# Performance work log

Hardware: AMD Instinct MI355X
Metric: run time of the kernel (lower is better)

Reference implementation:

```python
import jax, jax.numpy as jnp
import numpy as np
from jax import lax

B, T_ENC, T_DEC, D, MEL, PRE = 64, 300, 500, 512, 80, 256
K, C_LOC = 31, 32


def setup_inputs() -> dict:
    key = jax.random.key(0)
    ks = iter(jax.random.split(key, 40))
    def w(shape, s=0.05):
        return jax.random.normal(next(ks), shape, dtype=jnp.float32) * s
    zb = lambda n: jnp.zeros((n,), jnp.float32)
    return {
        "enc": w((B, T_ENC, D), 1.0),
        "mel_in": w((B, T_DEC, MEL), 1.0),
        "prenet_w1": w((PRE, MEL)), "prenet_b1": zb(PRE),
        "prenet_w2": w((PRE, PRE)), "prenet_b2": zb(PRE),
        "att_wih": w((4 * D, D + PRE)), "att_whh": w((4 * D, D)),
        "att_bih": zb(4 * D), "att_bhh": zb(4 * D),
        "dec_wih": w((4 * D, 2 * D)), "dec_whh": w((4 * D, D)),
        "dec_bih": zb(4 * D), "dec_bhh": zb(4 * D),
        "q_w": w((D, D)), "q_b": zb(D),
        "mem_w": w((D, D)), "mem_b": zb(D),
        "loc_conv_w": w((C_LOC, 2, K)), "loc_conv_b": zb(C_LOC),
        "loc_proj_w": w((D, C_LOC)), "loc_proj_b": zb(D),
        "v_w": w((1, D)), "v_b": zb(1),
        "mel_w": w((MEL, D)), "mel_b": zb(MEL),
        "stop_w": w((1, D)), "stop_b": zb(1),
    }


def _lstm(x, h, c, wih, whh, bih, bhh):
    # torch.nn.LSTMCell math: gates = x W_ih^T + b_ih + h W_hh^T + b_hh
    g = x @ wih.T + bih + h @ whh.T + bhh
    i, f, gg, o = jnp.split(g, 4, axis=-1)
    c = jax.nn.sigmoid(f) * c + jax.nn.sigmoid(i) * jnp.tanh(gg)
    h = jax.nn.sigmoid(o) * jnp.tanh(c)
    return h, c


def reference(enc, mel_in, prenet_w1, prenet_b1, prenet_w2, prenet_b2,
              att_wih, att_whh, att_bih, att_bhh,
              dec_wih, dec_whh, dec_bih, dec_bhh,
              q_w, q_b, mem_w, mem_b,
              loc_conv_w, loc_conv_b, loc_proj_w, loc_proj_b,
              v_w, v_b, mel_w, mel_b, stop_w, stop_b):
    # Eval mode (dropout/zoneout off), teacher_forcing=1.0 -> prev_mel = mel_in[:, t].
    Bb, T_enc, Dd = enc.shape
    pad = (loc_conv_w.shape[-1] - 1) // 2
    mproj = enc @ mem_w.T + mem_b  # [B, T_enc, D] (hoisted; constant across steps)

    def step(carry, prev_mel):
        ctx, a, a_cum, h_att, c_att, h_dec, c_dec = carry
        # prenet: two Linear+ReLU (dropout off in eval)
        pm = jax.nn.relu(jax.nn.relu(prev_mel @ prenet_w1.T + prenet_b1) @ prenet_w2.T + prenet_b2)
        h_att, c_att = _lstm(jnp.concatenate([pm, ctx], -1), h_att, c_att,
                             att_wih, att_whh, att_bih, att_bhh)
        # location-sensitive attention
        loc = jnp.stack([a, a_cum], axis=1)  # [B, 2, T_enc]
        conv = lax.conv_general_dilated(loc, loc_conv_w, (1,), [(pad, pad)],
                                        dimension_numbers=("NCH", "OIH", "NCH"))
        conv = conv + loc_conv_b[None, :, None]  # [B, C_loc, T_enc]
        loc_feat = jnp.einsum("bct,dc->btd", conv, loc_proj_w) + loc_proj_b  # [B, T_enc, D]
        q = (h_att @ q_w.T + q_b)[:, None, :]  # [B, 1, D]
        e = jnp.tanh(q + mproj + loc_feat) @ v_w[0] + v_b[0]  # [B, T_enc]
        a = jax.nn.softmax(e, axis=1)
        ctx = jnp.einsum("bt,btd->bd", a, enc)
        a_cum = a_cum + a
        h_dec, c_dec = _lstm(jnp.concatenate([h_att, ctx], -1), h_dec, c_dec,
                             dec_wih, dec_whh, dec_bih, dec_bhh)
        mel = h_dec @ mel_w.T + mel_b          # [B, mel_dim]
        stop = h_dec @ stop_w[0] + stop_b[0]   # [B]
        return (ctx, a, a_cum, h_att, c_att, h_dec, c_dec), (mel, stop)

    z = lambda *s: jnp.zeros(s, enc.dtype)
    init = (z(Bb, Dd), z(Bb, T_enc), z(Bb, T_enc), z(Bb, Dd), z(Bb, Dd), z(Bb, Dd), z(Bb, Dd))
    _, (mels, stops) = lax.scan(step, init, jnp.swapaxes(mel_in, 0, 1))
    mel_out = jnp.swapaxes(mels, 0, 1)    # [B, T_dec, mel_dim]
    stop_out = jnp.swapaxes(stops, 0, 1)  # [B, T_dec]
    return mel_out, stop_out
```

## Files before the change

### kernel.cpp

```cpp
#include <hip/hip_runtime.h>
#include <hip/hip_bf16.h>


#define DEV __device__ __forceinline__
typedef __hip_bfloat16 bf16;
DEV float b2f(bf16 x) { return __bfloat162float(x); }
DEV unsigned short f2us(float f) { bf16 h = __float2bfloat16(f); unsigned short u; __builtin_memcpy(&u, &h, 2); return u; }
DEV float us2f(unsigned short u) { union { float f; unsigned int i; } c; c.i = ((unsigned)u) << 16; return c.f; }

constexpr int NB = 256;

__device__ float g_enc[64*300*512];
__device__ __align__(16) float g_melT[500*80*64];
__device__ __align__(16) float g_w1[256*80];
__device__ float g_b1[256];
__device__ __align__(16) float g_w2[256*256];
__device__ float g_b2[256];
__device__ __align__(16) float g_awih[2048*768];
__device__ __align__(16) float g_awhh[2048*512];
__device__ float g_ab[2048];
__device__ __align__(16) float g_dwih[2048*1024];
__device__ __align__(16) float g_dwhh[2048*512];
__device__ float g_db[2048];
__device__ __align__(16) float g_qwt[512*512];
__device__ float g_qpb[512];
__device__ __align__(16) float g_memwt[512*512];
__device__ float g_memb[512];
__device__ float g_cw[32*62];
__device__ float g_cb[32];
__device__ __align__(16) float g_pw[512*32];
__device__ float g_vw[512];
__device__ __align__(16) float g_melw[80*512];
__device__ float g_melb[80];
__device__ __align__(16) float g_stopw[512];
__device__ float g_scal[2];
__device__ int   g_f32io;
__device__ __align__(16) float g_hatt4[2*512*64];
__device__ __align__(16) float g_hattT[64*512];
__device__ float g_catt[512*64];
__device__ __align__(16) float g_hdec4[2*512*64];
__device__ float g_cdec[512*64];
__device__ __align__(16) float g_ctx4[512*64];
__device__ float g_a[64*300];
__device__ float g_acum[64*300];
__device__ __align__(16) float g_pmt4[256*64];
__device__ __align__(16) float g_pm1t4[256*64];
__device__ float g_e[64*300];
__device__ int g_flag[NB*32];
__device__ int g_go[16*32];

struct InPtrs { const void* p[28]; };

DEV float sigf(float x) { return 1.f / (1.f + __expf(-x)); }
DEV float tanhf_fast(float x) {
  float e = __expf(-2.f * fabsf(x));
  float r = (1.f - e) / (1.f + e);
  return copysignf(r, x);
}
DEV int zero_vgpr() { int z; asm volatile("v_mov_b32 %0, 0" : "=v"(z)); return z; }

DEV float ald(const float* p) {
  return __hip_atomic_load(p, __ATOMIC_RELAXED, __HIP_MEMORY_SCOPE_AGENT);
}
DEV void ast(float* p, float v) {
  __hip_atomic_store(p, v, __ATOMIC_RELAXED, __HIP_MEMORY_SCOPE_AGENT);
}
DEV float2 ald2(const float* p) {
  unsigned long long u = __hip_atomic_load((const unsigned long long*)p,
                                           __ATOMIC_RELAXED, __HIP_MEMORY_SCOPE_AGENT);
  union { unsigned long long u; float2 f; } c; c.u = u; return c.f;
}

DEV int detect_f32(const void* enc_raw) {
  const unsigned short* u = (const unsigned short*)enc_raw;
  int big = 0;
  for (int i = 0; i < 256; i += 2) { int e = (u[i] >> 7) & 0xFF; big += (e > 133) ? 1 : 0; }
  return big >= 8 ? 1 : 0;
}
DEV float ldin(const void* p, int i, int f32) {
  return f32 ? ((const float*)p)[i] : b2f(((const bf16*)p)[i]);
}

__global__ __launch_bounds__(256) void k_convert(InPtrs P) {
  const int NT = gridDim.x * 256;
  const int flat = blockIdx.x * 256 + threadIdx.x;
  const int f32 = detect_f32(P.p[0]);
  if (flat == 0) {
    g_f32io = f32;
    g_scal[0] = ldin(P.p[23], 0, f32);
    g_scal[1] = ldin(P.p[27], 0, f32);
  }
#define CVT(dst, idx, n) for (int i = flat; i < (n); i += NT) dst[i] = ldin(P.p[idx], i, f32);
  CVT(g_enc, 0, 64*300*512)
  CVT(g_w1, 2, 256*80)   CVT(g_b1, 3, 256)
  CVT(g_w2, 4, 256*256)  CVT(g_b2, 5, 256)
  CVT(g_awih, 6, 2048*768)  CVT(g_awhh, 7, 2048*512)
  CVT(g_dwih, 10, 2048*1024) CVT(g_dwhh, 11, 2048*512)
  CVT(g_cw, 18, 32*62) CVT(g_cb, 19, 32)
  CVT(g_pw, 20, 512*32)  CVT(g_vw, 22, 512)
  CVT(g_melw, 24, 80*512) CVT(g_melb, 25, 80)
  CVT(g_stopw, 26, 512)  CVT(g_memb, 17, 512)
#undef CVT
  for (int i = flat; i < 500*80*64; i += NT) {
    int b = i & 63, tm = i >> 6;
    g_melT[i] = ldin(P.p[1], b*40000 + tm, f32);
  }
  for (int i = flat; i < 2048; i += NT) g_ab[i] = ldin(P.p[8], i, f32) + ldin(P.p[9], i, f32);
  for (int i = flat; i < 2048; i += NT) g_db[i] = ldin(P.p[12], i, f32) + ldin(P.p[13], i, f32);
  for (int i = flat; i < 512; i += NT) g_qpb[i] = ldin(P.p[15], i, f32) + ldin(P.p[21], i, f32);
  for (int o = flat; o < 512*512; o += NT) {
    int d = o >> 9, k = o & 511;
    g_memwt[(size_t)k*512 + d] = ldin(P.p[16], o, f32);
    g_qwt[(size_t)k*512 + d]   = ldin(P.p[14], o, f32);
  }
  for (int i = flat; i < 2*512*64; i += NT) { g_hatt4[i] = 0.f; g_hdec4[i] = 0.f; }
  for (int i = flat; i < 512*64; i += NT) { g_catt[i] = 0.f; g_cdec[i] = 0.f; g_ctx4[i] = 0.f; }
  for (int i = flat; i < 64*512; i += NT) g_hattT[i] = 0.f;
  for (int i = flat; i < 64*300; i += NT) { g_a[i] = 0.f; g_acum[i] = 0.f; }
  for (int i = flat; i < NB*32; i += NT) g_flag[i] = 0;
  for (int i = flat; i < 16*32; i += NT) g_go[i] = 0;
}

DEV void gbar(int n, int bb, int tid) {
  asm volatile("s_waitcnt vmcnt(0) lgkmcnt(0)" ::: "memory");
  __syncthreads();
  if (tid == 0)
    __hip_atomic_store(&g_flag[bb*32], n, __ATOMIC_RELAXED, __HIP_MEMORY_SCOPE_AGENT);
  if (bb == 0) {
    if (tid < 256)
      while (__hip_atomic_load(&g_flag[tid*32], __ATOMIC_RELAXED, __HIP_MEMORY_SCOPE_AGENT) < n)
        __builtin_amdgcn_s_sleep(1);
    __syncthreads();
    if (tid < 16)
      __hip_atomic_store(&g_go[tid*32], n, __ATOMIC_RELAXED, __HIP_MEMORY_SCOPE_AGENT);
  } else {
    if (tid == 0) {
      while (__hip_atomic_load(&g_go[(bb>>4)*32], __ATOMIC_RELAXED, __HIP_MEMORY_SCOPE_AGENT) < n)
        __builtin_amdgcn_s_sleep(1);
    }
  }
  __syncthreads();
}

template<int RS>
DEV void pdot16(const float* __restrict__ X4, const float* __restrict__ W0,
                int bbu, int k0, int nk, int lane, float* acc) {
#pragma unroll 2
  for (int k = k0; k < k0 + nk; k += 8) {
    const float* xp = X4 + k*64 + lane*4;
    float2 xa0 = ald2(xp);
    float2 xb0 = ald2(xp + 2);
    float2 xa1 = ald2(xp + 256);
    float2 xb1 = ald2(xp + 258);
#pragma unroll
    for (int g = 0; g < 4; ++g) {
#pragma unroll
      for (int u = 0; u < 4; ++u) {
        const float* wp = W0 + (size_t)(g*512 + bbu*4 + u)*RS + k;
        float4 w0 = *(const float4*)(wp);
        float4 w1 = *(const float4*)(wp + 4);
        float a = acc[g*4+u];
        a = fmaf(w0.x, xa0.x, a); a = fmaf(w0.y, xa0.y, a);
        a = fmaf(w0.z, xb0.x, a); a = fmaf(w0.w, xb0.y, a);
        a = fmaf(w1.x, xa1.x, a); a = fmaf(w1.y, xa1.y, a);
        a = fmaf(w1.z, xb1.x, a); a = fmaf(w1.w, xb1.y, a);
        acc[g*4+u] = a;
      }
    }
  }
}

DEV float dotSg(const float* __restrict__ X4, const float* __restrict__ wr,
                int n, int lane, float acc) {
#pragma unroll 2
  for (int k = 0; k < n; k += 8) {
    const float* xp = X4 + k*64 + lane*4;
    float2 xa0 = ald2(xp);
    float2 xb0 = ald2(xp + 2);
    float2 xa1 = ald2(xp + 256);
    float2 xb1 = ald2(xp + 258);
    float4 u0 = *(const float4*)(wr + k);
    float4 u1 = *(const float4*)(wr + k + 4);
    acc = fmaf(u0.x, xa0.x, acc); acc = fmaf(u0.y, xa0.y, acc);
    acc = fmaf(u0.z, xb0.x, acc); acc = fmaf(u0.w, xb0.y, acc);
    acc = fmaf(u1.x, xa1.x, acc); acc = fmaf(u1.y, xa1.y, acc);
    acc = fmaf(u1.z, xb1.x, acc); acc = fmaf(u1.w, xb1.y, acc);
  }
  return acc;
}

__global__ __launch_bounds__(512) void k_dec(void* outv) {
  const int bb = blockIdx.x;
  const int tid = threadIdx.x;
  const int lane = tid & 63, wv = tid >> 6;
  const int h = wv >> 2, dwv = wv & 3;
  const int f32io = g_f32io;
  const int zi = zero_vgpr();
  bf16* outh = (bf16*)outv;
  float* outf = (float*)outv;

  __shared__ __align__(16) float sbuf[8192];
  __shared__ float part[8][40];
  __shared__ float s_h[512];
  __shared__ float s_aa[664];
  __shared__ float s_cw[2016];

  const int eb = bb >> 2, tt0 = (bb & 3) * 75;
  const int da = dwv*128 + lane*2;
  const int r0 = h*38, nr = 38 - h;
  int bn = 0;

  for (int i = tid; i < 1984; i += 512) s_cw[i] = g_cw[i];
  for (int i = tid; i < 32; i += 512) s_cw[1984 + i] = g_cb[i];
  for (int i = tid; i < 664; i += 512) s_aa[i] = 0.f;
  __syncthreads();

  const int bbu = (bb < 128) ? bb : (bb - 128);
  const int jrow = bbu*4 + dwv;
  float bi, bfg, bgg, bog;
  if (bb < 128) { bi = g_ab[jrow]; bfg = g_ab[512+jrow]; bgg = g_ab[1024+jrow]; bog = g_ab[1536+jrow]; }
  else          { bi = g_db[jrow]; bfg = g_db[512+jrow]; bgg = g_db[1024+jrow]; bog = g_db[1536+jrow]; }
  float prb = 0.f;
  if (bb >= 128 && bb < 148) prb = g_melb[(bb-128)*4 + dwv];
  else if (bb >= 64 && bb < 128) prb = g_b2[(bb-64)*4 + dwv];
  else if (bb >= 192) prb = g_b1[(bb-192)*4 + dwv];

  if (bb >= 192 && tid < 256) {
    float acc = prb;
    const float* mt = g_melT + lane;
    const float* wr = g_w1 + zi + (size_t)((bb-192)*4 + dwv)*80;
#pragma unroll
    for (int m4 = 0; m4 < 20; ++m4) {
      float4 w = *(const float4*)(wr + m4*4);
      acc = fmaf(w.x, mt[(m4*4+0)*64], acc);
      acc = fmaf(w.y, mt[(m4*4+1)*64], acc);
      acc = fmaf(w.z, mt[(m4*4+2)*64], acc);
      acc = fmaf(w.w, mt[(m4*4+3)*64], acc);
    }
    ast(&g_pm1t4[(bb-192)*256 + lane*4 + dwv], fmaxf(acc, 0.f));
  }
  gbar(++bn, bb, tid);

  unsigned int mpq[38];
  {
    float a1[38], a2[38];
#pragma unroll
    for (int r = 0; r < 38; ++r) { a1[r] = 0.f; a2[r] = 0.f; }
    for (int kt = 0; kt < 16; ++kt) {
      __syncthreads();
      for (int i = tid; i < 75*32; i += 512) {
        int r = i >> 5, kk = i & 31;
        sbuf[i] = g_enc[((size_t)eb*300 + tt0 + r)*512 + kt*32 + kk];
      }
      __syncthreads();
      for (int kk = 0; kk < 32; ++kk) {
        const int k = kt*32 + kk;
        const float2 w = *(const float2*)(g_memwt + (size_t)k*512 + da);
#pragma unroll
        for (int r = 0; r < 38; ++r) {
          const float ev = sbuf[(r0 + r)*32 + kk];
          a1[r] = fmaf(ev, w.x, a1[r]);
          a2[r] = fmaf(ev, w.y, a2[r]);
        }
      }
    }
    const float2 mb = *(const float2*)(g_memb + da);
#pragma unroll
    for (int r = 0; r < 38; ++r)
      mpq[r] = (unsigned)f2us(a1[r] + mb.x) | ((unsigned)f2us(a2[r] + mb.y) << 16);
    if (bb >= 64 && bb < 128 && wv < 4) {
      float acc = dotSg(g_pm1t4, g_w2 + zi + (size_t)((bb-64)*4 + dwv)*256, 256, lane, prb);
      ast(&g_pmt4[(bb-64)*256 + lane*4 + dwv], fmaxf(acc, 0.f));
    }
  }
  float Pa[32], Pb[32];
#pragma unroll
  for (int i = 0; i < 8; ++i) {
    float4 u = *(const float4*)(g_pw + (size_t)da*32 + 4*i);
    float4 w = *(const float4*)(g_pw + (size_t)(da+1)*32 + 4*i);
    Pa[4*i] = u.x; Pa[4*i+1] = u.y; Pa[4*i+2] = u.z; Pa[4*i+3] = u.w;
    Pb[4*i] = w.x; Pb[4*i+1] = w.y; Pb[4*i+2] = w.z; Pb[4*i+3] = w.w;
  }
  const float2 vv  = *(const float2*)(g_vw + da);
  const float2 qb2 = *(const float2*)(g_qpb + da);
  const float v1 = vv.x, v2 = vv.y;
  const float vb = g_scal[0];
  gbar(++bn, bb, tid);

  for (int t = 0; t <= 500; ++t) {
    const int rp = t & 1, wp = rp ^ 1;

    if (bb < 128) {
      if (t < 500) {
        float acc[16];
#pragma unroll
        for (int r = 0; r < 16; ++r) acc[r] = 0.f;
        pdot16<768>(g_pmt4, g_awih + zi, bb, wv*32, 32, lane, acc);
        pdot16<768>(g_ctx4, g_awih + zi + 256, bb, wv*64, 64, lane, acc);
        pdot16<512>(g_hatt4 + rp*(512*64), g_awhh + zi, bb, wv*64, 64, lane, acc);
#pragma unroll
        for (int r = 0; r < 16; ++r) sbuf[r*512 + wv*64 + lane] = acc[r];
        __syncthreads();
        if (wv < 4) {
          float s0 = bi, s1 = bfg, s2 = bgg, s3 = bog;
#pragma unroll
          for (int w = 0; w < 8; ++w) {
            s0 += sbuf[(dwv)*512      + w*64 + lane];
            s1 += sbuf[(4 + dwv)*512  + w*64 + lane];
            s2 += sbuf[(8 + dwv)*512  + w*64 + lane];
            s3 += sbuf[(12 + dwv)*512 + w*64 + lane];
          }
          const float c = g_catt[jrow*64 + lane];
          const float cn = sigf(s1)*c + sigf(s0)*tanhf_fast(s2);
          const float hn = sigf(s3)*tanhf_fast(cn);
          g_catt[jrow*64 + lane] = cn;
          ast(&g_hatt4[wp*(512*64) + bb*256 + lane*4 + dwv], hn);
          ast(&g_hattT[lane*512 + jrow], hn);
        }
      }
    } else {
      if (t > 0) {
        float acc[16];
#pragma unroll
        for (int r = 0; r < 16; ++r) acc[r] = 0.f;
        pdot16<1024>(g_hatt4 + rp*(512*64), g_dwih + zi, bbu, wv*64, 64, lane, acc);
        pdot16<1024>(g_ctx4, g_dwih + zi + 512, bbu, wv*64, 64, lane, acc);
        pdot16<512>(g_hdec4 + wp*(512*64), g_dwhh + zi, bbu, wv*64, 64, lane, acc);
#pragma unroll
        for (int r = 0; r < 16; ++r) sbuf[r*512 + wv*64 + lane] = acc[r];
        __syncthreads();
        if (wv < 4) {
          float s0 = bi, s1 = bfg, s2 = bgg, s3 = bog;
#pragma unroll
          for (int w = 0; w < 8; ++w) {
            s0 += sbuf[(dwv)*512      + w*64 + lane];
            s1 += sbuf[(4 + dwv)*512  + w*64 + lane];
            s2 += sbuf[(8 + dwv)*512  + w*64 + lane];
            s3 += sbuf[(12 + dwv)*512 + w*64 + lane];
          }
          const float c = g_cdec[jrow*64 + lane];
          const float cn = sigf(s1)*c + sigf(s0)*tanhf_fast(s2);
          const float hn = sigf(s3)*tanhf_fast(cn);
          g_cdec[jrow*64 + lane] = cn;
          ast(&g_hdec4[rp*(512*64) + (bb-128)*256 + lane*4 + dwv], hn);
        }
      }
    }
    gbar(++bn, bb, tid);

    if (t < 500) {
      s_h[tid] = ald(&g_hattT[eb*512 + tid]);
      if (tid < 300) {
        s_aa[15 + tid]  = ald(&g_a[eb*300 + tid]);
        s_aa[347 + tid] = ald(&g_acum[eb*300 + tid]);
      }
      __syncthreads();
      for (int i = tid; i < 75*32; i += 512) {
        const int ttl = i >> 5, c2 = i & 31;
        const int tt = tt0 + ttl;
        float s = s_cw[1984 + c2];
#pragma unroll
        for (int k = 0; k < 31; ++k) {
          s = fmaf(s_cw[c2*62 + k],      s_aa[tt + k], s);
          s = fmaf(s_cw[c2*62 + 31 + k], s_aa[332 + tt + k], s);
        }
        sbuf[i] = s;
      }
      float q1p = h ? 0.f : qb2.x, q2p = h ? 0.f : qb2.y;
      {
        const int kb = h*256;
#pragma unroll 8
        for (int k = kb; k < kb + 256; k += 2) {
          const float h0 = s_h[k], h1 = s_h[k+1];
          const float2 wA = *(const float2*)(g_qwt + (size_t)k*512 + da);
          const float2 wB = *(const float2*)(g_qwt + (size_t)(k+1)*512 + da);
          q1p = fmaf(wA.x, h0, q1p); q2p = fmaf(wA.y, h0, q2p);
          q1p = fmaf(wB.x, h1, q1p); q2p = fmaf(wB.y, h1, q2p);
        }
      }
      float2* qp = (float2*)(sbuf + 4096);
      qp[wv*64 + lane] = make_float2(q1p, q2p);
      __syncthreads();
      const float2 qA = qp[dwv*64 + lane];
      const float2 qB = qp[(4 + dwv)*64 + lane];
      const float q1 = qA.x + qB.x, q2 = qA.y + qB.y;
#pragma unroll
      for (int i = 0; i < 38; ++i) {
        if (i < nr) {
          const int gi = r0 + i;
          float s1 = q1 + us2f((unsigned short)(mpq[i] & 0xffffu));
          float s2 = q2 + us2f((unsigned short)(mpq[i] >> 16));
          const float4* cr = (const float4*)(sbuf + gi*32);
#pragma unroll
          for (int c4 = 0; c4 < 8; ++c4) {
            const float4 cv = cr[c4];
            s1 = fmaf(Pa[c4*4+0], cv.x, s1); s2 = fmaf(Pb[c4*4+0], cv.x, s2);
            s1 = fmaf(Pa[c4*4+1], cv.y, s1); s2 = fmaf(Pb[c4*4+1], cv.y, s2);
            s1 = fmaf(Pa[c4*4+2], cv.z, s1); s2 = fmaf(Pb[c4*4+2], cv.z, s2);
            s1 = fmaf(Pa[c4*4+3], cv.w, s1); s2 = fmaf(Pb[c4*4+3], cv.w, s2);
          }
          float p = v1*tanhf_fast(s1) + v2*tanhf_fast(s2);
#pragma unroll
          for (int m = 32; m >= 1; m >>= 1) p += __shfl_xor(p, m, 64);
          if (lane == 0) part[wv][i] = p;
        }
      }
      __syncthreads();
      if (tid < 75) {
        float e;
        if (tid < 38) e = part[0][tid] + part[1][tid] + part[2][tid] + part[3][tid];
        else          e = part[4][tid-38] + part[5][tid-38] + part[6][tid-38] + part[7][tid-38];
        ast(&g_e[eb*300 + tt0 + tid], e + vb);
      }
    }
    if (t <= 498 && bb >= 192 && tid < 256) {
      float acc = prb;
      const float* mt = g_melT + (size_t)(t+1)*5120 + lane;
      const float* wr = g_w1 + zi + (size_t)((bb-192)*4 + dwv)*80;
#pragma unroll
      for (int m4 = 0; m4 < 20; ++m4) {
        float4 w = *(const float4*)(wr + m4*4);
        acc = fmaf(w.x, mt[(m4*4+0)*64], acc);
        acc = fmaf(w.y, mt[(m4*4+1)*64], acc);
        acc = fmaf(w.z, mt[(m4*4+2)*64], acc);
        acc = fmaf(w.w, mt[(m4*4+3)*64], acc);
      }
      ast(&g_pm1t4[(bb-192)*256 + lane*4 + dwv], fmaxf(acc, 0.f));
    }
    gbar(++bn, bb, tid);

    if (t < 500) {
      if (bb < 64) {
        float* pl = sbuf; float* red = sbuf + 304;
        const int b_ = bb;
        const float* Ep = g_e + b_*300;
        const float e1 = (tid < 300) ? ald(Ep + tid) : -3e38f;
        red[tid] = e1; __syncthreads();
        for (int s = 256; s > 0; s >>= 1) { if (tid < s) red[tid] = fmaxf(red[tid], red[tid+s]); __syncthreads(); }
        const float mx = red[0]; __syncthreads();
        const float p1 = (tid < 300) ? __expf(e1 - mx) : 0.f;
        if (tid < 300) pl[tid] = p1;
        red[tid] = p1; __syncthreads();
        for (int s = 256; s > 0; s >>= 1) { if (tid < s) red[tid] += red[tid+s]; __syncthreads(); }
        const float inv = 1.f / red[0];
        if (tid < 300) {
          const float av = p1*inv;
          const float oc = ald(&g_acum[b_*300 + tid]);
          ast(&g_a[b_*300 + tid], av);
          ast(&g_acum[b_*300 + tid], oc + av);
        }
        __syncthreads();
        const float* ep = g_enc + (size_t)(b_*300)*512;
        const int dd = tid;
        float acc = 0.f;
#pragma unroll 8
        for (int tt = 0; tt < 300; ++tt) acc = fmaf(pl[tt], ep[(size_t)tt*512 + dd], acc);
        ast(&g_ctx4[(dd >> 2)*256 + b_*4 + (dd & 3)], acc * inv);
      } else if (bb < 128) {
        if (t <= 498 && wv < 4) {
          float acc = dotSg(g_pm1t4, g_w2 + zi + (size_t)((bb-64)*4 + dwv)*256, 256, lane, prb);
          ast(&g_pmt4[(bb-64)*256 + lane*4 + dwv], fmaxf(acc, 0.f));
        }
      }
    }
    if (t > 0 && bb >= 128 && bb < 148 && wv < 4) {
      float acc = dotSg(g_hdec4 + rp*(512*64),
                        g_melw + zi + (size_t)((bb-128)*4 + dwv)*512, 512, lane, prb);
      const int m = (bb-128)*4 + dwv;
      const size_t oidx = (size_t)(lane*500 + (t-1))*80 + m;
      if (f32io) outf[oidx] = acc; else outh[oidx] = __float2bfloat16(acc);
    } else if (t > 0 && bb == 148 && tid < 64) {
      float acc = dotSg(g_hdec4 + rp*(512*64), g_stopw + zi, 512, tid, g_scal[1]);
      const size_t oidx = 2560000 + tid*500 + (t-1);
      if (f32io) outf[oidx] = acc; else outh[oidx] = __float2bfloat16(acc);
    }
    gbar(++bn, bb, tid);
  }
}

extern "C" void kernel_launch(void* const* d_in, const int* in_sizes, int n_in,
                              void* d_out, int out_size, void* d_ws, size_t ws_size,
                              hipStream_t stream) {
  (void)d_ws; (void)ws_size; (void)in_sizes; (void)out_size;
  InPtrs P;
  for (int i = 0; i < 28 && i < n_in; ++i) P.p[i] = d_in[i];
  k_convert<<<dim3(2048), dim3(256), 0, stream>>>(P);
  k_dec<<<dim3(NB), dim3(512), 0, stream>>>(d_out);
}
```

Before: 111.0 ms.

## Batch x-vector loads in LSTM dots, tile location conv, pipeline context loads

Several micro-optimizations to the persistent decoder kernel. pdot16 now loads all x chunks up front (fully unrolled) before the FMA loop, so more memory requests are in flight. The location conv is register-tiled with 5 outputs per thread, and the attention-weight smem loads are hoisted before the LSTM phase. The context reduction double-buffers the encoder loads with two accumulators. Removing the zero_vgpr trick lets weight pointers become scalar again, and the q projection uses float2 LDS loads. The cost is higher register pressure that could reduce occupancy or cause spills.

Result: slower. 200.5 ms (+80.7%).

```diff
diff --git a/kernel.cpp b/kernel.cpp
--- a/kernel.cpp
+++ b/kernel.cpp
@@ -57,7 +57,6 @@
   float r = (1.f - e) / (1.f + e);
   return copysignf(r, x);
 }
-DEV int zero_vgpr() { int z; asm volatile("v_mov_b32 %0, 0" : "=v"(z)); return z; }
 
 DEV float ald(const float* p) {
   return __hip_atomic_load(p, __ATOMIC_RELAXED, __HIP_MEMORY_SCOPE_AGENT);
@@ -142,16 +141,21 @@
   __syncthreads();
 }
 
-template<int RS>
+template<int RS, int NC>
 DEV void pdot16(const float* __restrict__ X4, const float* __restrict__ W0,
-                int bbu, int k0, int nk, int lane, float* acc) {
-#pragma unroll 2
-  for (int k = k0; k < k0 + nk; k += 8) {
-    const float* xp = X4 + k*64 + lane*4;
-    float2 xa0 = ald2(xp);
-    float2 xb0 = ald2(xp + 2);
-    float2 xa1 = ald2(xp + 256);
-    float2 xb1 = ald2(xp + 258);
+                int bbu, int k0, int lane, float* acc) {
+  float2 xr[NC*4];
+#pragma unroll
+  for (int c = 0; c < NC; ++c) {
+    const float* xp = X4 + (k0 + c*8)*64 + lane*4;
+    xr[c*4+0] = ald2(xp);
+    xr[c*4+1] = ald2(xp + 2);
+    xr[c*4+2] = ald2(xp + 256);
+    xr[c*4+3] = ald2(xp + 258);
+  }
+#pragma unroll
+  for (int c = 0; c < NC; ++c) {
+    const int k = k0 + c*8;
 #pragma unroll
     for (int g = 0; g < 4; ++g) {
 #pragma unroll
@@ -160,10 +164,10 @@
         float4 w0 = *(const float4*)(wp);
         float4 w1 = *(const float4*)(wp + 4);
         float a = acc[g*4+u];
-        a = fmaf(w0.x, xa0.x, a); a = fmaf(w0.y, xa0.y, a);
-        a = fmaf(w0.z, xb0.x, a); a = fmaf(w0.w, xb0.y, a);
-        a = fmaf(w1.x, xa1.x, a); a = fmaf(w1.y, xa1.y, a);
-        a = fmaf(w1.z, xb1.x, a); a = fmaf(w1.w, xb1.y, a);
+        a = fmaf(w0.x, xr[c*4+0].x, a); a = fmaf(w0.y, xr[c*4+0].y, a);
+        a = fmaf(w0.z, xr[c*4+1].x, a); a = fmaf(w0.w, xr[c*4+1].y, a);
+        a = fmaf(w1.x, xr[c*4+2].x, a); a = fmaf(w1.y, xr[c*4+2].y, a);
+        a = fmaf(w1.z, xr[c*4+3].x, a); a = fmaf(w1.w, xr[c*4+3].y, a);
         acc[g*4+u] = a;
       }
     }
@@ -195,14 +199,13 @@
   const int lane = tid & 63, wv = tid >> 6;
   const int h = wv >> 2, dwv = wv & 3;
   const int f32io = g_f32io;
-  const int zi = zero_vgpr();
   bf16* outh = (bf16*)outv;
   float* outf = (float*)outv;
 
   __shared__ __align__(16) float sbuf[8192];
   __shared__ float part[8][40];
   __shared__ float s_h[512];
-  __shared__ float s_aa[664];
+  __shared__ float s_aa[704];
   __shared__ float s_cw[2016];
 
   const int eb = bb >> 2, tt0 = (bb & 3) * 75;
@@ -212,7 +215,7 @@
 
   for (int i = tid; i < 1984; i += 512) s_cw[i] = g_cw[i];
   for (int i = tid; i < 32; i += 512) s_cw[1984 + i] = g_cb[i];
-  for (int i = tid; i < 664; i += 512) s_aa[i] = 0.f;
+  for (int i = tid; i < 704; i += 512) s_aa[i] = 0.f;
   __syncthreads();
 
   const int bbu = (bb < 128) ? bb : (bb - 128);
@@ -228,7 +231,7 @@
   if (bb >= 192 && tid < 256) {
     float acc = prb;
     const float* mt = g_melT + lane;
-    const float* wr = g_w1 + zi + (size_t)((bb-192)*4 + dwv)*80;
+    const float* wr = g_w1 + (size_t)((bb-192)*4 + dwv)*80;
 #pragma unroll
     for (int m4 = 0; m4 < 20; ++m4) {
       float4 w = *(const float4*)(wr + m4*4);
@@ -269,7 +272,7 @@
     for (int r = 0; r < 38; ++r)
       mpq[r] = (unsigned)f2us(a1[r] + mb.x) | ((unsigned)f2us(a2[r] + mb.y) << 16);
     if (bb >= 64 && bb < 128 && wv < 4) {
-      float acc = dotSg(g_pm1t4, g_w2 + zi + (size_t)((bb-64)*4 + dwv)*256, 256, lane, prb);
+      float acc = dotSg(g_pm1t4, g_w2 + (size_t)((bb-64)*4 + dwv)*256, 256, lane, prb);
       ast(&g_pmt4[(bb-64)*256 + lane*4 + dwv], fmaxf(acc, 0.f));
     }
   }
@@ -290,14 +293,18 @@
   for (int t = 0; t <= 500; ++t) {
     const int rp = t & 1, wp = rp ^ 1;
 
+    if (t < 500 && tid < 300) {
+      s_aa[15 + tid]  = ald(&g_a[eb*300 + tid]);
+      s_aa[347 + tid] = ald(&g_acum[eb*300 + tid]);
+    }
     if (bb < 128) {
       if (t < 500) {
         float acc[16];
 #pragma unroll
         for (int r = 0; r < 16; ++r) acc[r] = 0.f;
-        pdot16<768>(g_pmt4, g_awih + zi, bb, wv*32, 32, lane, acc);
-        pdot16<768>(g_ctx4, g_awih + zi + 256, bb, wv*64, 64, lane, acc);
-        pdot16<512>(g_hatt4 + rp*(512*64), g_awhh + zi, bb, wv*64, 64, lane, acc);
+        pdot16<768,4>(g_pmt4, g_awih, bb, wv*32, lane, acc);
+        pdot16<768,8>(g_ctx4, g_awih + 256, bb, wv*64, lane, acc);
+        pdot16<512,8>(g_hatt4 + rp*(512*64), g_awhh, bb, wv*64, lane, acc);
 #pragma unroll
         for (int r = 0; r < 16; ++r) sbuf[r*512 + wv*64 + lane] = acc[r];
         __syncthreads();
@@ -323,9 +330,9 @@
         float acc[16];
 #pragma unroll
         for (int r = 0; r < 16; ++r) acc[r] = 0.f;
-        pdot16<1024>(g_hatt4 + rp*(512*64), g_dwih + zi, bbu, wv*64, 64, lane, acc);
-        pdot16<1024>(g_ctx4, g_dwih + zi + 512, bbu, wv*64, 64, lane, acc);
-        pdot16<512>(g_hdec4 + wp*(512*64), g_dwhh + zi, bbu, wv*64, 64, lane, acc);
+        pdot16<1024,8>(g_hatt4 + rp*(512*64), g_dwih, bbu, wv*64, lane, acc);
+        pdot16<1024,8>(g_ctx4, g_dwih + 512, bbu, wv*64, lane, acc);
+        pdot16<512,8>(g_hdec4 + wp*(512*64), g_dwhh, bbu, wv*64, lane, acc);
 #pragma unroll
         for (int r = 0; r < 16; ++r) sbuf[r*512 + wv*64 + lane] = acc[r];
         __syncthreads();
@@ -350,32 +357,39 @@
 
     if (t < 500) {
       s_h[tid] = ald(&g_hattT[eb*512 + tid]);
-      if (tid < 300) {
-        s_aa[15 + tid]  = ald(&g_a[eb*300 + tid]);
-        s_aa[347 + tid] = ald(&g_acum[eb*300 + tid]);
-      }
       __syncthreads();
-      for (int i = tid; i < 75*32; i += 512) {
-        const int ttl = i >> 5, c2 = i & 31;
-        const int tt = tt0 + ttl;
-        float s = s_cw[1984 + c2];
-#pragma unroll
+      {
+        const int c2 = tid & 31, tb = tid >> 5;
+        const float cb0 = s_cw[1984 + c2];
+        float sc[5];
+#pragma unroll
+        for (int j = 0; j < 5; ++j) sc[j] = cb0;
         for (int k = 0; k < 31; ++k) {
-          s = fmaf(s_cw[c2*62 + k],      s_aa[tt + k], s);
-          s = fmaf(s_cw[c2*62 + 31 + k], s_aa[332 + tt + k], s);
-        }
-        sbuf[i] = s;
+          const float w1 = s_cw[c2*62 + k];
+          const float w2 = s_cw[c2*62 + 31 + k];
+          const int base = tt0 + tb + k;
+#pragma unroll
+          for (int j = 0; j < 5; ++j) {
+            sc[j] = fmaf(w1, s_aa[base + 16*j], sc[j]);
+            sc[j] = fmaf(w2, s_aa[332 + base + 16*j], sc[j]);
+          }
+        }
+#pragma unroll
+        for (int j = 0; j < 5; ++j) {
+          const int row = tb + 16*j;
+          if (row < 75) sbuf[row*32 + c2] = sc[j];
+        }
       }
       float q1p = h ? 0.f : qb2.x, q2p = h ? 0.f : qb2.y;
       {
         const int kb = h*256;
 #pragma unroll 8
         for (int k = kb; k < kb + 256; k += 2) {
-          const float h0 = s_h[k], h1 = s_h[k+1];
+          const float2 hh = *(const float2*)(s_h + k);
           const float2 wA = *(const float2*)(g_qwt + (size_t)k*512 + da);
           const float2 wB = *(const float2*)(g_qwt + (size_t)(k+1)*512 + da);
-          q1p = fmaf(wA.x, h0, q1p); q2p = fmaf(wA.y, h0, q2p);
-          q1p = fmaf(wB.x, h1, q1p); q2p = fmaf(wB.y, h1, q2p);
+          q1p = fmaf(wA.x, hh.x, q1p); q2p = fmaf(wA.y, hh.x, q2p);
+          q1p = fmaf(wB.x, hh.y, q1p); q2p = fmaf(wB.y, hh.y, q2p);
         }
       }
       float2* qp = (float2*)(sbuf + 4096);
@@ -416,7 +430,7 @@
     if (t <= 498 && bb >= 192 && tid < 256) {
       float acc = prb;
       const float* mt = g_melT + (size_t)(t+1)*5120 + lane;
-      const float* wr = g_w1 + zi + (size_t)((bb-192)*4 + dwv)*80;
+      const float* wr = g_w1 + (size_t)((bb-192)*4 + dwv)*80;
 #pragma unroll
       for (int m4 = 0; m4 < 20; ++m4) {
         float4 w = *(const float4*)(wr + m4*4);
@@ -450,27 +464,39 @@
           ast(&g_acum[b_*300 + tid], oc + av);
         }
         __syncthreads();
-        const float* ep = g_enc + (size_t)(b_*300)*512;
-        const int dd = tid;
-        float acc = 0.f;
-#pragma unroll 8
-        for (int tt = 0; tt < 300; ++tt) acc = fmaf(pl[tt], ep[(size_t)tt*512 + dd], acc);
-        ast(&g_ctx4[(dd >> 2)*256 + b_*4 + (dd & 3)], acc * inv);
+        const float* ep = g_enc + (size_t)(b_*300)*512 + tid;
+        float eA[10], eB[10];
+        float ac0 = 0.f, ac1 = 0.f;
+#pragma unroll
+        for (int i = 0; i < 10; ++i) eA[i] = ep[(size_t)i*512];
+        for (int tt = 0; tt < 300; tt += 20) {
+#pragma unroll
+          for (int i = 0; i < 10; ++i) eB[i] = ep[(size_t)(tt+10+i)*512];
+#pragma unroll
+          for (int i = 0; i < 10; ++i) ac0 = fmaf(pl[tt+i], eA[i], ac0);
+          if (tt + 20 < 300) {
+#pragma unroll
+            for (int i = 0; i < 10; ++i) eA[i] = ep[(size_t)(tt+20+i)*512];
+          }
+#pragma unroll
+          for (int i = 0; i < 10; ++i) ac1 = fmaf(pl[tt+10+i], eB[i], ac1);
+        }
+        ast(&g_ctx4[(tid >> 2)*256 + b_*4 + (tid & 3)], (ac0 + ac1) * inv);
       } else if (bb < 128) {
         if (t <= 498 && wv < 4) {
-          float acc = dotSg(g_pm1t4, g_w2 + zi + (size_t)((bb-64)*4 + dwv)*256, 256, lane, prb);
+          float acc = dotSg(g_pm1t4, g_w2 + (size_t)((bb-64)*4 + dwv)*256, 256, lane, prb);
           ast(&g_pmt4[(bb-64)*256 + lane*4 + dwv], fmaxf(acc, 0.f));
         }
       }
     }
     if (t > 0 && bb >= 128 && bb < 148 && wv < 4) {
       float acc = dotSg(g_hdec4 + rp*(512*64),
-                        g_melw + zi + (size_t)((bb-128)*4 + dwv)*512, 512, lane, prb);
+                        g_melw + (size_t)((bb-128)*4 + dwv)*512, 512, lane, prb);
       const int m = (bb-128)*4 + dwv;
       const size_t oidx = (size_t)(lane*500 + (t-1))*80 + m;
       if (f32io) outf[oidx] = acc; else outh[oidx] = __float2bfloat16(acc);
     } else if (t > 0 && bb == 148 && tid < 64) {
-      float acc = dotSg(g_hdec4 + rp*(512*64), g_stopw + zi, 512, tid, g_scal[1]);
+      float acc = dotSg(g_hdec4 + rp*(512*64), g_stopw, 512, tid, g_scal[1]);
       const size_t oidx = 2560000 + tid*500 + (t-1);
       if (f32io) outf[oidx] = acc; else outh[oidx] = __float2bfloat16(acc);
     }
```
